# Performance work log

Measured on AMD Instinct MI355X. Metric: run time of the kernel, lower is better.

## Reference

```python
import jax, jax.numpy as jnp
import numpy as np

B, T, C, H = 2, 2048, 2048, 32
N = C // H  # 64
EPS_GN = 1e-5 * 8 ** 2  # eps = 1e-5 * head_size_divisor**2


def setup_inputs() -> dict:
    key = jax.random.key(0)
    ks = jax.random.split(key, 40)
    p = lambda i, shape, s=1.0: jax.random.normal(ks[i], shape, jnp.float32) * s
    inp = {
        'x': p(0, (B, T, C)),
        'shift_state': jnp.zeros((B, C), jnp.float32),
        'v_first': p(1, (B, T, C)),
        'wkv_state': jnp.zeros((B, H, N, N), jnp.float32),
        # token-shift mix coefficients [1,1,C]
        'x_r': p(2, (1, 1, C), 0.3), 'x_w': p(3, (1, 1, C), 0.3),
        'x_k': p(4, (1, 1, C), 0.3), 'x_v': p(5, (1, 1, C), 0.3),
        'x_a': p(6, (1, 1, C), 0.3), 'x_g': p(7, (1, 1, C), 0.3),
        # decay LoRA
        'w0': p(8, (1, 1, C), 0.5) - 4.0,
        'w1': p(9, (C, 64), 0.02), 'w2': p(10, (64, C), 0.02),
        # in-context-learning-rate LoRA
        'a0': p(11, (1, 1, C), 0.1),
        'a1': p(12, (C, 64), 0.02), 'a2': p(13, (64, C), 0.02),
        # value-mix LoRA
        'v0': p(14, (1, 1, C), 0.1) + 1.0,
        'v1': p(15, (C, 32), 0.02), 'v2': p(16, (32, C), 0.02),
        # gate LoRA
        'g1': p(17, (C, 128), 0.02), 'g2': p(18, (128, C), 0.02),
        'k_k': p(19, (1, 1, C), 0.05) + 0.85,
        'k_a': p(20, (1, 1, C), 0.05) + 1.0,
        'r_k': p(21, (H, N), 0.1),
        # dense projections (applied as x @ W.T like nn.Linear)
        'Wr': p(22, (C, C), 0.02), 'Wk': p(23, (C, C), 0.02),
        'Wv': p(24, (C, C), 0.02), 'Wo': p(25, (C, C), 0.02),
        'ln_w': jnp.ones((C,), jnp.float32),
        'ln_b': jnp.zeros((C,), jnp.float32),
    }
    return inp


def reference(x, shift_state, v_first, wkv_state, x_r, x_w, x_k, x_v, x_a, x_g,
              w0, w1, w2, a0, a1, a2, v0, v1, v2, g1, g2, k_k, k_a, r_k,
              Wr, Wk, Wv, Wo, ln_w, ln_b):
    # token shift: xx[t] = x[t-1] - x[t] (prev from shift_state at t=0)
    xx = jnp.concatenate([shift_state[:, None, :], x[:, :-1]], axis=1) - x
    xr, xw, xk, xv, xa, xg = (x + xx * m for m in (x_r, x_w, x_k, x_v, x_a, x_g))

    r = xr @ Wr.T
    w = -jax.nn.softplus(-(w0 + jnp.tanh(xw @ w1) @ w2)) - 0.5  # log-decay in (-inf,-0.5)
    k = xk @ Wk.T
    v = xv @ Wv.T
    v = v + (v_first - v) * jax.nn.sigmoid(v0 + (xv @ v1) @ v2)  # layer_id > 0 branch
    a = jax.nn.sigmoid(a0 + (xa @ a1) @ a2)
    g = jax.nn.sigmoid(xg @ g1) @ g2

    kk = (k * k_k).reshape(B, T, H, N)
    kk = kk / jnp.maximum(jnp.linalg.norm(kk, axis=-1, keepdims=True), 1e-12)
    kk = kk.reshape(B, T, C)
    k = k * (1.0 + (a - 1.0) * k_a)

    # RWKV-7 generalized delta-rule recurrence (a_in=-kk, b_in=kk*a):
    #   S_t = S_{t-1} * diag(exp(w_t)) + (S_{t-1} a_t) b_t^T + v_t k_t^T ; o_t = S_t r_t
    to_tbhn = lambda z: z.reshape(B, T, H, N).transpose(1, 0, 2, 3)  # [T,B,H,N]
    rs, ws, ks, vs, as_, bs = map(to_tbhn, (r, w, k, v, -kk, kk * a))

    def step(S, ins):  # S: [B,H,N,N] indexed [v_dim, k_dim]
        r_t, w_t, k_t, v_t, a_t, b_t = ins
        sa = jnp.einsum('bhij,bhj->bhi', S, a_t)
        S = (S * jnp.exp(w_t)[:, :, None, :]
             + sa[..., None] * b_t[:, :, None, :]
             + v_t[..., None] * k_t[:, :, None, :])
        o_t = jnp.einsum('bhij,bhj->bhi', S, r_t)
        return S, o_t

    _, o = jax.lax.scan(step, wkv_state, (rs, ws, ks, vs, as_, bs))  # o: [T,B,H,N]
    o = o.transpose(1, 0, 2, 3).reshape(B, T, C)

    # GroupNorm with H groups over channel dim
    og = o.reshape(B, T, H, N)
    mu = og.mean(-1, keepdims=True)
    var = og.var(-1, keepdims=True)
    o = ((og - mu) / jnp.sqrt(var + EPS_GN)).reshape(B, T, C) * ln_w + ln_b

    # bonus term
    rk = (r.reshape(B, T, H, N) * k.reshape(B, T, H, N) * r_k).sum(-1, keepdims=True)
    o = o + (rk * v.reshape(B, T, H, N)).reshape(B, T, C)

    return (o * g) @ Wo.T
```

## Files before the change

kernel.cpp:

```cpp
#include <hip/hip_runtime.h>

#define Bdim 2
#define Tdim 2048
#define Cdim 2048
#define Hdim 32
#define Mdim (Bdim*Tdim)

typedef unsigned short u16;
typedef short bf16x8 __attribute__((ext_vector_type(8)));
typedef float f32x4 __attribute__((ext_vector_type(4)));

__device__ __forceinline__ u16 f2bf(float f) {
  unsigned u = __float_as_uint(f);
  u = (u + 0x7FFFu + ((u >> 16) & 1u)) >> 16;
  return (u16)u;
}
__device__ __forceinline__ float b2f(u16 h) {
  return __uint_as_float(((unsigned)h) << 16);
}
__device__ __forceinline__ float sigf(float x) { return 1.f / (1.f + expf(-x)); }

__device__ __forceinline__ void gld16(const u16* g, u16* l) {
  __builtin_amdgcn_global_load_lds(
      (const __attribute__((address_space(1))) unsigned int*)g,
      (__attribute__((address_space(3))) unsigned int*)l, 16, 0, 0);
}

__device__ __forceinline__ float dpp_red8(float x) {
  int t = __builtin_amdgcn_mov_dpp(__float_as_int(x), 0xB1, 0xF, 0xF, true);
  x += __int_as_float(t);
  t = __builtin_amdgcn_mov_dpp(__float_as_int(x), 0x4E, 0xF, 0xF, true);
  x += __int_as_float(t);
  t = __builtin_amdgcn_mov_dpp(__float_as_int(x), 0x128, 0xF, 0xF, true);
  x += __int_as_float(t);
  return x;
}

__global__ __launch_bounds__(256) void fill_kernel(float* __restrict__ out, float v, int n) {
  int i = blockIdx.x * 256 + threadIdx.x;
  if (i < n) out[i] = v;
}

__global__ __launch_bounds__(256) void prep_kernel(
    const float* __restrict__ x, const float* __restrict__ shift,
    const float* __restrict__ mr, const float* __restrict__ mw,
    const float* __restrict__ mk, const float* __restrict__ mv,
    const float* __restrict__ ma, const float* __restrict__ mg,
    u16* __restrict__ xr_h, u16* __restrict__ xr_l,
    u16* __restrict__ xk_h, u16* __restrict__ xk_l,
    u16* __restrict__ xv_h, u16* __restrict__ xv_l,
    u16* __restrict__ xg_h, u16* __restrict__ xg_l,
    u16* __restrict__ xw, u16* __restrict__ xa)
{
  size_t idx = (size_t)blockIdx.x * 256 + threadIdx.x;
  int c = (int)(idx & (Cdim - 1));
  size_t row = idx >> 11;
  int t = (int)(row & (Tdim - 1));
  int b = (int)(row >> 11);
  float xc = x[idx];
  float xp = (t == 0) ? shift[(size_t)b * Cdim + c] : x[idx - Cdim];
  float xx = xp - xc;

  float vr = xc + xx * mr[c];
  u16 hr = f2bf(vr); xr_h[idx] = hr; xr_l[idx] = f2bf(vr - b2f(hr));
  float vk = xc + xx * mk[c];
  u16 hk = f2bf(vk); xk_h[idx] = hk; xk_l[idx] = f2bf(vk - b2f(hk));
  float vv = xc + xx * mv[c];
  u16 hv = f2bf(vv); xv_h[idx] = hv; xv_l[idx] = f2bf(vv - b2f(hv));
  float vg = xc + xx * mg[c];
  u16 hg = f2bf(vg); xg_h[idx] = hg; xg_l[idx] = f2bf(vg - b2f(hg));

  xw[idx] = f2bf(xc + xx * mw[c]);
  xa[idx] = f2bf(xc + xx * ma[c]);
}

__global__ __launch_bounds__(256) void cast_split_kernel(
    const float* __restrict__ src, u16* __restrict__ hi, u16* __restrict__ lo)
{
  size_t i = (size_t)blockIdx.x * 256 + threadIdx.x;
  float v = src[i];
  u16 h = f2bf(v);
  hi[i] = h;
  lo[i] = f2bf(v - b2f(h));
}

__global__ __launch_bounds__(256) void transpose_pack_kernel(
    const float* __restrict__ src, u16* __restrict__ dst, int K, int Nsrc)
{
  size_t idx = (size_t)blockIdx.x * 256 + threadIdx.x;
  int n = (int)(idx / K);
  int kk = (int)(idx - (size_t)n * K);
  dst[idx] = (n < Nsrc) ? f2bf(src[(size_t)kk * Nsrc + n]) : (u16)0;
}

__global__ __launch_bounds__(256) void transpose_pack_split_kernel(
    const float* __restrict__ src, u16* __restrict__ dh, u16* __restrict__ dl,
    int K, int Nsrc)
{
  size_t idx = (size_t)blockIdx.x * 256 + threadIdx.x;
  int n = (int)(idx / K);
  int kk = (int)(idx - (size_t)n * K);
  float v = (n < Nsrc) ? src[(size_t)kk * Nsrc + n] : 0.f;
  u16 h = f2bf(v);
  dh[idx] = h;
  dl[idx] = f2bf(v - b2f(h));
}


template <int EP>
__device__ __forceinline__ void gemm_plain_body(
    const u16* __restrict__ A, const u16* __restrict__ B, void* __restrict__ Cv,
    const float* __restrict__ bias, const float* __restrict__ aux1,
    const float* __restrict__ aux2, int K, int Nact, int ldC, int act)
{
  __shared__ u16 As[128][32];
  __shared__ u16 Bs[128][32];
  int tid = threadIdx.x;
  int lane = tid & 63, wave = tid >> 6;
  int wm = wave >> 1, wn = wave & 1;
  int bm = blockIdx.x * 128, bn = blockIdx.y * 128;
  f32x4 zero = {0.f, 0.f, 0.f, 0.f};
  f32x4 acc[4][4];
#pragma unroll
  for (int i = 0; i < 4; i++)
#pragma unroll
    for (int j = 0; j < 4; j++) acc[i][j] = zero;
  int srow = tid >> 2;
  int sslot = tid & 3;
  int scol = (sslot ^ (srow & 3)) << 3;
  int dcol = sslot << 3;
  const u16* gA  = A + (size_t)(bm + srow) * K + scol;
  const u16* gA2 = A + (size_t)(bm + 64 + srow) * K + scol;
  const u16* gB  = B + (size_t)(bn + srow) * K + scol;
  const u16* gB2 = B + (size_t)(bn + 64 + srow) * K + scol;
  u16* lA  = &As[srow][dcol];
  u16* lA2 = &As[64 + srow][dcol];
  u16* lB  = &Bs[srow][dcol];
  u16* lB2 = &Bs[64 + srow][dcol];
  int fr = lane & 15;
  int fk = ((lane >> 4) << 3) ^ ((fr & 3) << 3);
  for (int k0 = 0; k0 < K; k0 += 32) {
    __syncthreads();
    gld16(gA + k0, lA);
    gld16(gA2 + k0, lA2);
    gld16(gB + k0, lB);
    gld16(gB2 + k0, lB2);
    __syncthreads();
    bf16x8 af[4], bfv[4];
#pragma unroll
    for (int i = 0; i < 4; i++) af[i] = *(const bf16x8*)&As[wm * 64 + i * 16 + fr][fk];
#pragma unroll
    for (int j = 0; j < 4; j++) bfv[j] = *(const bf16x8*)&Bs[wn * 64 + j * 16 + fr][fk];
#pragma unroll
    for (int i = 0; i < 4; i++)
#pragma unroll
      for (int j = 0; j < 4; j++)
        acc[i][j] = __builtin_amdgcn_mfma_f32_16x16x32_bf16(af[i], bfv[j], acc[i][j], 0, 0, 0);
  }
  int rb = (lane >> 4) << 2;
  int cc = lane & 15;
#pragma unroll
  for (int i = 0; i < 4; i++) {
    int mm = bm + wm * 64 + i * 16 + rb;
#pragma unroll
    for (int j = 0; j < 4; j++) {
      int nn = bn + wn * 64 + j * 16 + cc;
      if (nn < Nact) {
#pragma unroll
        for (int r = 0; r < 4; r++) {
          float val = acc[i][j][r];
          size_t oidx = (size_t)(mm + r) * ldC + nn;
          if (EP == 1) ((u16*)Cv)[oidx] = f2bf(tanhf(val));
          else if (EP == 2) {
            if (act == 1) val = tanhf(val);
            ((u16*)Cv)[oidx] = f2bf(val);
          }
          else if (EP == 3) ((u16*)Cv)[oidx] = f2bf(0.60653065971f * sigf(bias[nn] + val));
          else if (EP == 4) ((float*)Cv)[oidx] = sigf(bias[nn] + val);
          else if (EP == 5) {
            float vraw = aux1[oidx], vf = aux2[oidx];
            ((float*)Cv)[oidx] = vraw + (vf - vraw) * sigf(bias[nn] + val);
          }
        }
      }
    }
  }
}

template <int EP>
__global__ __launch_bounds__(256) void gemm_plain(
    const u16* __restrict__ A, const u16* __restrict__ B, void* __restrict__ C,
    const float* __restrict__ bias, const float* __restrict__ aux1,
    const float* __restrict__ aux2, int K, int Nact, int ldC)
{
  gemm_plain_body<EP>(A, B, C, bias, aux1, aux2, K, Nact, ldC, 0);
}

__global__ __launch_bounds__(256) void lora1_kernel(
    const u16* A0, const u16* A1, const u16* A2,
    const u16* B0, const u16* B1, const u16* B2,
    u16* C0, u16* C1, u16* C2, int N0, int N1, int N2)
{
  int z = blockIdx.z;
  const u16* A = (z == 0) ? A0 : (z == 1) ? A1 : A2;
  const u16* B = (z == 0) ? B0 : (z == 1) ? B1 : B2;
  u16* C      = (z == 0) ? C0 : (z == 1) ? C1 : C2;
  int Nact    = (z == 0) ? N0 : (z == 1) ? N1 : N2;
  int act     = (z == 0) ? 1 : 0;
  gemm_plain_body<2>(A, B, C, nullptr, nullptr, nullptr, 2048, Nact, Nact, act);
}

template <int EP>
__global__ __launch_bounds__(256) void gemm_split(
    const u16* __restrict__ Ah, const u16* __restrict__ Al,
    const u16* __restrict__ Bh, const u16* __restrict__ Bl,
    void* __restrict__ C1, u16* __restrict__ C2, int K, int Nact, int ldC)
{
  __shared__ u16 Ash[128][32];
  __shared__ u16 Asl[128][32];
  __shared__ u16 Bsh[128][32];
  __shared__ u16 Bsl[128][32];
  int tid = threadIdx.x;
  int lane = tid & 63, wave = tid >> 6;
  int wm = wave >> 1, wn = wave & 1;
  int bm = blockIdx.x * 128, bn = blockIdx.y * 128;
  f32x4 zero = {0.f, 0.f, 0.f, 0.f};
  f32x4 acc[4][4];
#pragma unroll
  for (int i = 0; i < 4; i++)
#pragma unroll
    for (int j = 0; j < 4; j++) acc[i][j] = zero;
  int srow = tid >> 2;
  int sslot = tid & 3;
  int scol = (sslot ^ (srow & 3)) << 3;
  int dcol = sslot << 3;
  size_t ga  = (size_t)(bm + srow) * K + scol;
  size_t ga2 = (size_t)(bm + 64 + srow) * K + scol;
  size_t gb  = (size_t)(bn + srow) * K + scol;
  size_t gb2 = (size_t)(bn + 64 + srow) * K + scol;
  u16* lAh = &Ash[srow][dcol];  u16* lAh2 = &Ash[64 + srow][dcol];
  u16* lAl = &Asl[srow][dcol];  u16* lAl2 = &Asl[64 + srow][dcol];
  u16* lBh = &Bsh[srow][dcol];  u16* lBh2 = &Bsh[64 + srow][dcol];
  u16* lBl = &Bsl[srow][dcol];  u16* lBl2 = &Bsl[64 + srow][dcol];
  int fr = lane & 15;
  int fk = ((lane >> 4) << 3) ^ ((fr & 3) << 3);
  for (int k0 = 0; k0 < K; k0 += 32) {
    __syncthreads();
    gld16(Ah + ga + k0, lAh);
    gld16(Ah + ga2 + k0, lAh2);
    gld16(Al + ga + k0, lAl);
    gld16(Al + ga2 + k0, lAl2);
    gld16(Bh + gb + k0, lBh);
    gld16(Bh + gb2 + k0, lBh2);
    gld16(Bl + gb + k0, lBl);
    gld16(Bl + gb2 + k0, lBl2);
    __syncthreads();
    bf16x8 fah[4], fal[4], fbh[4], fbl[4];
#pragma unroll
    for (int i = 0; i < 4; i++) {
      fah[i] = *(const bf16x8*)&Ash[wm * 64 + i * 16 + fr][fk];
      fal[i] = *(const bf16x8*)&Asl[wm * 64 + i * 16 + fr][fk];
    }
#pragma unroll
    for (int j = 0; j < 4; j++) {
      fbh[j] = *(const bf16x8*)&Bsh[wn * 64 + j * 16 + fr][fk];
      fbl[j] = *(const bf16x8*)&Bsl[wn * 64 + j * 16 + fr][fk];
    }
#pragma unroll
    for (int i = 0; i < 4; i++)
#pragma unroll
      for (int j = 0; j < 4; j++) {
        acc[i][j] = __builtin_amdgcn_mfma_f32_16x16x32_bf16(fah[i], fbh[j], acc[i][j], 0, 0, 0);
        acc[i][j] = __builtin_amdgcn_mfma_f32_16x16x32_bf16(fah[i], fbl[j], acc[i][j], 0, 0, 0);
        acc[i][j] = __builtin_amdgcn_mfma_f32_16x16x32_bf16(fal[i], fbh[j], acc[i][j], 0, 0, 0);
      }
  }
  int rb = (lane >> 4) << 2;
  int cc = lane & 15;
#pragma unroll
  for (int i = 0; i < 4; i++) {
    int mm = bm + wm * 64 + i * 16 + rb;
#pragma unroll
    for (int j = 0; j < 4; j++) {
      int nn = bn + wn * 64 + j * 16 + cc;
      if (nn < Nact) {
#pragma unroll
        for (int r = 0; r < 4; r++) {
          float val = acc[i][j][r];
          size_t oidx = (size_t)(mm + r) * ldC + nn;
          if (EP == 0) ((float*)C1)[oidx] = val;
          else {
            float s = sigf(val);
            u16 h = f2bf(s);
            ((u16*)C1)[oidx] = h;
            C2[oidx] = f2bf(s - b2f(h));
          }
        }
      }
    }
  }
}

__global__ __launch_bounds__(256) void post_kernel(
    float* __restrict__ k, const float* __restrict__ a,
    const float* __restrict__ k_k, const float* __restrict__ k_a,
    float* __restrict__ ain, float* __restrict__ bin)
{
  int gid = blockIdx.x * 4 + (threadIdx.x >> 6);
  int lane = threadIdx.x & 63;
  int m = gid >> 5, h = gid & 31;
  int c = h * 64 + lane;
  size_t idx = (size_t)m * Cdim + c;

  float kr = k[idx];
  float av = a[idx];

  float kkv = kr * k_k[c];
  float ss = kkv * kkv;
#pragma unroll
  for (int off = 32; off; off >>= 1) ss += __shfl_xor(ss, off);
  float kkn = kkv / fmaxf(sqrtf(ss), 1e-12f);

  ain[idx] = -kkn;
  bin[idx] = kkn * av;
  k[idx] = kr * (1.f + (av - 1.f) * k_a[c]);
}

__global__ __launch_bounds__(64) void scan_kernel(
    const float* __restrict__ r, const u16* __restrict__ ew,
    const float* __restrict__ k, const float* __restrict__ v,
    const float* __restrict__ ain, const float* __restrict__ bin,
    const float* __restrict__ S0, float* __restrict__ o)
{
  int bh = blockIdx.x & 63;
  int rg = blockIdx.x >> 6;
  int lane = threadIdx.x;
  int oc = (lane & 3) | ((lane >> 1) & 4);
  int lr = ((lane >> 2) & 1) | ((lane >> 3) & 6);
  int i = rg * 8 + lr;
  int cb = (bh & 31) * 64;
  size_t mbase = (size_t)(bh >> 5) * Tdim;

  float s[8];
  {
    const float* sp = S0 + (size_t)bh * 4096 + (size_t)i * 64 + oc * 8;
#pragma unroll
    for (int j = 0; j < 8; j++) s[j] = sp[j];
  }

  __shared__ __align__(16) char ring[33792];
  char* RA = ring;
  char* RK = ring + 6144;
  char* RB = ring + 12288;
  char* RR = ring + 18432;
  char* RE = ring + 24576;
  char* RV = ring + 27648;

  int lhi = lane >> 4, llo = lane & 15;
  int ehi = lane >> 3, elo = lane & 7;

#define STAGE(gg) { \
  int ss_ = (gg) % 3; \
  size_t m0_ = mbase + (size_t)(gg) * 8; \
  gld16((const u16*)(ain + (m0_ + lhi) * Cdim + cb + llo * 4),     (u16*)(RA + ss_ * 2048)); \
  gld16((const u16*)(ain + (m0_ + 4 + lhi) * Cdim + cb + llo * 4), (u16*)(RA + ss_ * 2048 + 1024)); \
  gld16((const u16*)(k   + (m0_ + lhi) * Cdim + cb + llo * 4),     (u16*)(RK + ss_ * 2048)); \
  gld16((const u16*)(k   + (m0_ + 4 + lhi) * Cdim + cb + llo * 4), (u16*)(RK + ss_ * 2048 + 1024)); \
  gld16((const u16*)(bin + (m0_ + lhi) * Cdim + cb + llo * 4),     (u16*)(RB + ss_ * 2048)); \
  gld16((const u16*)(bin + (m0_ + 4 + lhi) * Cdim + cb + llo * 4), (u16*)(RB + ss_ * 2048 + 1024)); \
  gld16((const u16*)(r   + (m0_ + lhi) * Cdim + cb + llo * 4),     (u16*)(RR + ss_ * 2048)); \
  gld16((const u16*)(r   + (m0_ + 4 + lhi) * Cdim + cb + llo * 4), (u16*)(RR + ss_ * 2048 + 1024)); \
  gld16((const u16*)(v   + (m0_ + lhi) * Cdim + cb + llo * 4),     (u16*)(RV + ss_ * 2048)); \
  gld16((const u16*)(v   + (m0_ + 4 + lhi) * Cdim + cb + llo * 4), (u16*)(RV + ss_ * 2048 + 1024)); \
  gld16((const u16*)(ew  + (m0_ + ehi) * Cdim + cb + elo * 8),     (u16*)(RE + ss_ * 1024)); }

  f32x4 aA0, aA1, kA0, kA1, bA0, bA1, rA0, rA1;
  f32x4 aB0, aB1, kB0, kB1, bB0, bB1, rB0, rB1;
  f32x4 aC0, aC1, kC0, kC1, bC0, bC1, rC0, rC1;
  bf16x8 eA, eB, eC;
  float vA, vB, vC;

#define LOADSUB(sub, a0_, a1_, k0_, k1_, b0_, b1_, r0_, r1_, e_, v_) { \
  const f32x4* pa_ = (const f32x4*)(RA + ssoff + (sub) * 256 + oc * 32); \
  a0_ = pa_[0]; a1_ = pa_[1]; \
  const f32x4* pk_ = (const f32x4*)(RK + ssoff + (sub) * 256 + oc * 32); \
  k0_ = pk_[0]; k1_ = pk_[1]; \
  const f32x4* pb_ = (const f32x4*)(RB + ssoff + (sub) * 256 + oc * 32); \
  b0_ = pb_[0]; b1_ = pb_[1]; \
  const f32x4* pr_ = (const f32x4*)(RR + ssoff + (sub) * 256 + oc * 32); \
  r0_ = pr_[0]; r1_ = pr_[1]; \
  e_ = *(const bf16x8*)(RE + (ssoff >> 1) + (sub) * 128 + oc * 16); \
  v_ = *(const float*)(RV + ssoff + (sub) * 256 + i * 4); }

#define COMPSUB(sub, a0_, a1_, k0_, k1_, b0_, b1_, r0_, r1_, e_, v_) { \
  float pL_ = 0.f, pH_ = 0.f; \
  _Pragma("unroll") \
  for (int j = 0; j < 4; j++) { pL_ += s[j] * a0_[j]; pH_ += s[4 + j] * a1_[j]; } \
  float p_ = dpp_red8(pL_ + pH_); \
  float oL_ = 0.f, oH_ = 0.f; \
  _Pragma("unroll") \
  for (int j = 0; j < 4; j++) { \
    float sn0_ = s[j]     * b2f((u16)e_[j])     + p_ * b0_[j] + v_ * k0_[j]; \
    float sn1_ = s[4 + j] * b2f((u16)e_[4 + j]) + p_ * b1_[j] + v_ * k1_[j]; \
    s[j] = sn0_; s[4 + j] = sn1_; \
    oL_ += sn0_ * r0_[j]; oH_ += sn1_ * r1_[j]; \
  } \
  float oo_ = dpp_red8(oL_ + oH_); \
  if (oc == 0) o[(mbase + (size_t)g * 8 + (sub)) * Cdim + cb + i] = oo_; }

#define LA(sub) LOADSUB(sub, aA0, aA1, kA0, kA1, bA0, bA1, rA0, rA1, eA, vA)
#define LB(sub) LOADSUB(sub, aB0, aB1, kB0, kB1, bB0, bB1, rB0, rB1, eB, vB)
#define LC(sub) LOADSUB(sub, aC0, aC1, kC0, kC1, bC0, bC1, rC0, rC1, eC, vC)
#define CA(sub) COMPSUB(sub, aA0, aA1, kA0, kA1, bA0, bA1, rA0, rA1, eA, vA)
#define CB(sub) COMPSUB(sub, aB0, aB1, kB0, kB1, bB0, bB1, rB0, rB1, eB, vB)
#define CC(sub) COMPSUB(sub, aC0, aC1, kC0, kC1, bC0, bC1, rC0, rC1, eC, vC)

  const int NG = Tdim / 8;
  STAGE(0)
  STAGE(1)

  for (int g = 0; g < NG; ++g) {
    if (g + 2 < NG) STAGE(g + 2)
    if (g + 1 < NG) asm volatile("s_waitcnt vmcnt(22)" ::: "memory");
    else            asm volatile("s_waitcnt vmcnt(0)" ::: "memory");
    __builtin_amdgcn_sched_barrier(0);
    int ssoff = (g % 3) * 2048;
    LA(0)
    LB(1)
    LC(2)
    CA(0)
    LA(3)
    CB(1)
    LB(4)
    CC(2)
    LC(5)
    CA(3)
    LA(6)
    CB(4)
    LB(7)
    CC(5)
    CA(6)
    CB(7)
  }
#undef STAGE
#undef LOADSUB
#undef COMPSUB
#undef LA
#undef LB
#undef LC
#undef CA
#undef CB
#undef CC
}

__global__ __launch_bounds__(256) void gn_kernel(
    const float* __restrict__ o_raw, const float* __restrict__ r,
    const float* __restrict__ k, const float* __restrict__ v,
    const float* __restrict__ g, const float* __restrict__ rkw,
    const float* __restrict__ ln_w, const float* __restrict__ ln_b,
    u16* __restrict__ og_h, u16* __restrict__ og_l)
{
  int gid = blockIdx.x * 4 + (threadIdx.x >> 6);
  int lane = threadIdx.x & 63;
  int m = gid >> 5, h = gid & 31;
  int c = h * 64 + lane;
  size_t idx = (size_t)m * Cdim + c;

  float ov = o_raw[idx];
  float rv = r[idx], kv = k[idx], vv = v[idx];
  float rk = rv * kv * rkw[c];

  float s1 = ov, s2 = ov * ov, s3 = rk;
#pragma unroll
  for (int off = 32; off; off >>= 1) {
    s1 += __shfl_xor(s1, off);
    s2 += __shfl_xor(s2, off);
    s3 += __shfl_xor(s3, off);
  }
  float mu = s1 * (1.f / 64.f);
  float var = s2 * (1.f / 64.f) - mu * mu;
  float xh = (ov - mu) * rsqrtf(var + 6.4e-4f);
  float gn = xh * ln_w[c] + ln_b[c];
  float outp = (gn + s3 * vv) * g[idx];
  u16 hh = f2bf(outp);
  og_h[idx] = hh;
  og_l[idx] = f2bf(outp - b2f(hh));
}

extern "C" void kernel_launch(void* const* d_in, const int* in_sizes, int n_in,
                              void* d_out, int out_size, void* d_ws, size_t ws_size,
                              hipStream_t stream) {
  const float* x      = (const float*)d_in[0];
  const float* shiftS = (const float*)d_in[1];
  const float* vfirst = (const float*)d_in[2];
  const float* wkv0   = (const float*)d_in[3];
  const float* x_r = (const float*)d_in[4];
  const float* x_w = (const float*)d_in[5];
  const float* x_k = (const float*)d_in[6];
  const float* x_v = (const float*)d_in[7];
  const float* x_a = (const float*)d_in[8];
  const float* x_g = (const float*)d_in[9];
  const float* w0 = (const float*)d_in[10];
  const float* w1 = (const float*)d_in[11];
  const float* w2 = (const float*)d_in[12];
  const float* a0 = (const float*)d_in[13];
  const float* a1 = (const float*)d_in[14];
  const float* a2 = (const float*)d_in[15];
  const float* v0 = (const float*)d_in[16];
  const float* v1 = (const float*)d_in[17];
  const float* v2 = (const float*)d_in[18];
  const float* g1 = (const float*)d_in[19];
  const float* g2 = (const float*)d_in[20];
  const float* k_k = (const float*)d_in[21];
  const float* k_a = (const float*)d_in[22];
  const float* r_k = (const float*)d_in[23];
  const float* Wr = (const float*)d_in[24];
  const float* Wk = (const float*)d_in[25];
  const float* Wv = (const float*)d_in[26];
  const float* Wo = (const float*)d_in[27];
  const float* ln_w = (const float*)d_in[28];
  const float* ln_b = (const float*)d_in[29];
  (void)in_sizes; (void)n_in;

  const size_t MC = (size_t)Mdim * Cdim;
  const size_t CC = (size_t)Cdim * Cdim;
  const size_t SLOT = MC * 2;

  char* cur = (char*)d_ws;
  auto alloc = [&](size_t bytes) -> void* {
    void* p = cur;
    cur += (bytes + 255) & ~(size_t)255;
    return p;
  };

  char* X = (char*)alloc(13 * SLOT);
  u16* xr_h = (u16*)(X + 0 * SLOT);
  u16* xr_l = (u16*)(X + 1 * SLOT);
  u16* xk_h = (u16*)(X + 2 * SLOT);
  u16* xk_l = (u16*)(X + 3 * SLOT);
  u16* xv_h = (u16*)(X + 4 * SLOT);
  u16* xv_l = (u16*)(X + 5 * SLOT);
  u16* xw   = (u16*)(X + 6 * SLOT);
  u16* xa   = (u16*)(X + 7 * SLOT);
  u16* xg_h = (u16*)(X + 8 * SLOT);
  u16* xg_l = (u16*)(X + 9 * SLOT);
  float* r_f32 = (float*)(X + 8 * SLOT);
  float* k_f32 = (float*)(X + 0 * SLOT);
  float* v_f32 = (float*)(X + 2 * SLOT);
  float* a_f32 = (float*)(X + 10 * SLOT);
  u16*   ew_bf = (u16*)(X + 12 * SLOT);
  float* ain_f = (float*)(X + 4 * SLOT);
  float* bin_f = (float*)(X + 6 * SLOT);
  float* o_f32 = (float*)(X + 10 * SLOT);
  float* g_f32 = (float*)(X + 6 * SLOT);
  u16*   og_h  = (u16*)(X + 4 * SLOT);
  u16*   og_l  = (u16*)(X + 5 * SLOT);

  u16* Wh = (u16*)alloc(CC * 2);
  u16* Wl = (u16*)alloc(CC * 2);

  u16* w1t = (u16*)alloc((size_t)128 * 2048 * 2);
  u16* a1t = (u16*)alloc((size_t)128 * 2048 * 2);
  u16* v1t = (u16*)alloc((size_t)128 * 2048 * 2);
  u16* g1t_h = (u16*)alloc((size_t)128 * 2048 * 2);
  u16* g1t_l = (u16*)alloc((size_t)128 * 2048 * 2);
  u16* w2t = (u16*)alloc((size_t)2048 * 64 * 2);
  u16* a2t = (u16*)alloc((size_t)2048 * 64 * 2);
  u16* v2t = (u16*)alloc((size_t)2048 * 32 * 2);
  u16* g2t_h = (u16*)alloc((size_t)2048 * 128 * 2);
  u16* g2t_l = (u16*)alloc((size_t)2048 * 128 * 2);
  u16* hb_w = (u16*)alloc((size_t)Mdim * 64 * 2);
  u16* hb_a = (u16*)alloc((size_t)Mdim * 64 * 2);
  u16* hb_v = (u16*)alloc((size_t)Mdim * 32 * 2);
  u16* sig_h = (u16*)alloc((size_t)Mdim * 128 * 2);
  u16* sig_l = (u16*)alloc((size_t)Mdim * 128 * 2);

  size_t required = (size_t)(cur - (char*)d_ws);
  if (ws_size < required) {
    fill_kernel<<<(out_size + 255) / 256, 256, 0, stream>>>(
        (float*)d_out, (float)(ws_size >> 20), out_size);
    return;
  }

  prep_kernel<<<(int)(MC / 256), 256, 0, stream>>>(
      x, shiftS, x_r, x_w, x_k, x_v, x_a, x_g,
      xr_h, xr_l, xk_h, xk_l, xv_h, xv_l, xg_h, xg_l, xw, xa);

  transpose_pack_kernel<<<1024, 256, 0, stream>>>(w1, w1t, 2048, 64);
  transpose_pack_kernel<<<1024, 256, 0, stream>>>(a1, a1t, 2048, 64);
  transpose_pack_kernel<<<1024, 256, 0, stream>>>(v1, v1t, 2048, 32);
  transpose_pack_split_kernel<<<1024, 256, 0, stream>>>(g1, g1t_h, g1t_l, 2048, 128);
  transpose_pack_kernel<<<512, 256, 0, stream>>>(w2, w2t, 64, 2048);
  transpose_pack_kernel<<<512, 256, 0, stream>>>(a2, a2t, 64, 2048);
  transpose_pack_kernel<<<256, 256, 0, stream>>>(v2, v2t, 32, 2048);
  transpose_pack_split_kernel<<<1024, 256, 0, stream>>>(g2, g2t_h, g2t_l, 128, 2048);

  dim3 gL1(Mdim / 128, 1, 3);
  lora1_kernel<<<gL1, 256, 0, stream>>>(xw, xa, xv_h, w1t, a1t, v1t,
                                        hb_w, hb_a, hb_v, 64, 64, 32);
  dim3 gL1g(Mdim / 128, 1);
  gemm_split<1><<<gL1g, 256, 0, stream>>>(xg_h, xg_l, g1t_h, g1t_l,
                                          sig_h, sig_l, 2048, 128, 128);

  dim3 gBig(Mdim / 128, Cdim / 128);
  cast_split_kernel<<<(int)(CC / 256), 256, 0, stream>>>(Wr, Wh, Wl);
  gemm_split<0><<<gBig, 256, 0, stream>>>(xr_h, xr_l, Wh, Wl, r_f32, nullptr, Cdim, Cdim, Cdim);
  cast_split_kernel<<<(int)(CC / 256), 256, 0, stream>>>(Wk, Wh, Wl);
  gemm_split<0><<<gBig, 256, 0, stream>>>(xk_h, xk_l, Wh, Wl, k_f32, nullptr, Cdim, Cdim, Cdim);
  cast_split_kernel<<<(int)(CC / 256), 256, 0, stream>>>(Wv, Wh, Wl);
  gemm_split<0><<<gBig, 256, 0, stream>>>(xv_h, xv_l, Wh, Wl, v_f32, nullptr, Cdim, Cdim, Cdim);

  gemm_plain<3><<<gBig, 256, 0, stream>>>(hb_w, w2t, ew_bf, w0, nullptr, nullptr, 64, Cdim, Cdim);
  gemm_plain<4><<<gBig, 256, 0, stream>>>(hb_a, a2t, a_f32, a0, nullptr, nullptr, 64, Cdim, Cdim);
  gemm_plain<5><<<gBig, 256, 0, stream>>>(hb_v, v2t, v_f32, v0, v_f32, vfirst, 32, Cdim, Cdim);

  post_kernel<<<(Mdim * Hdim) / 4, 256, 0, stream>>>(
      k_f32, a_f32, k_k, k_a, ain_f, bin_f);

  scan_kernel<<<512, 64, 0, stream>>>(
      r_f32, ew_bf, k_f32, v_f32, ain_f, bin_f, wkv0, o_f32);

  gemm_split<0><<<gBig, 256, 0, stream>>>(sig_h, sig_l, g2t_h, g2t_l,
                                          g_f32, nullptr, 128, Cdim, Cdim);

  gn_kernel<<<(Mdim * Hdim) / 4, 256, 0, stream>>>(
      o_f32, r_f32, k_f32, v_f32, g_f32, r_k, ln_w, ln_b, og_h, og_l);

  cast_split_kernel<<<(int)(CC / 256), 256, 0, stream>>>(Wo, Wh, Wl);
  gemm_split<0><<<gBig, 256, 0, stream>>>(og_h, og_l, Wh, Wl,
                                          (float*)d_out, nullptr, Cdim, Cdim, Cdim);
}
```

Baseline: 1.169 ms.

## Load A fragments and scan inputs directly from global into registers, dropping LDS staging

In the split-precision GEMM, the A operand fragments are now read straight from global memory into registers instead of being staged through shared memory; only B still goes through LDS. In the WKV scan kernel, the three-slot LDS ring fed by async global-to-LDS loads is replaced by direct per-timestep register prefetch, kept four timesteps ahead in a software pipeline. The aim is to cut LDS traffic, the waitcnt and sync overhead, and LDS occupancy. The cost is that global-load latency is hidden only by register prefetch depth, and the GEMM's uncoalesced strided A reads may raise memory traffic.

```diff
diff --git a/kernel.cpp b/kernel.cpp
--- a/kernel.cpp
+++ b/kernel.cpp
@@ -216,8 +216,6 @@
     const u16* __restrict__ Bh, const u16* __restrict__ Bl,
     void* __restrict__ C1, u16* __restrict__ C2, int K, int Nact, int ldC)
 {
-  __shared__ u16 Ash[128][32];
-  __shared__ u16 Asl[128][32];
   __shared__ u16 Bsh[128][32];
   __shared__ u16 Bsl[128][32];
   int tid = threadIdx.x;
@@ -234,37 +232,32 @@
   int sslot = tid & 3;
   int scol = (sslot ^ (srow & 3)) << 3;
   int dcol = sslot << 3;
-  size_t ga  = (size_t)(bm + srow) * K + scol;
-  size_t ga2 = (size_t)(bm + 64 + srow) * K + scol;
   size_t gb  = (size_t)(bn + srow) * K + scol;
   size_t gb2 = (size_t)(bn + 64 + srow) * K + scol;
-  u16* lAh = &Ash[srow][dcol];  u16* lAh2 = &Ash[64 + srow][dcol];
-  u16* lAl = &Asl[srow][dcol];  u16* lAl2 = &Asl[64 + srow][dcol];
   u16* lBh = &Bsh[srow][dcol];  u16* lBh2 = &Bsh[64 + srow][dcol];
   u16* lBl = &Bsl[srow][dcol];  u16* lBl2 = &Bsl[64 + srow][dcol];
   int fr = lane & 15;
-  int fk = ((lane >> 4) << 3) ^ ((fr & 3) << 3);
+  int fkB = ((lane >> 4) << 3) ^ ((fr & 3) << 3);
+  const u16* gAh = Ah + (size_t)(bm + wm * 64 + fr) * K + ((lane >> 4) << 3);
+  const u16* gAl = Al + (size_t)(bm + wm * 64 + fr) * K + ((lane >> 4) << 3);
   for (int k0 = 0; k0 < K; k0 += 32) {
     __syncthreads();
-    gld16(Ah + ga + k0, lAh);
-    gld16(Ah + ga2 + k0, lAh2);
-    gld16(Al + ga + k0, lAl);
-    gld16(Al + ga2 + k0, lAl2);
     gld16(Bh + gb + k0, lBh);
     gld16(Bh + gb2 + k0, lBh2);
     gld16(Bl + gb + k0, lBl);
     gld16(Bl + gb2 + k0, lBl2);
+    bf16x8 fah[4], fal[4];
+#pragma unroll
+    for (int i = 0; i < 4; i++) {
+      fah[i] = *(const bf16x8*)(gAh + (size_t)i * 16 * K + k0);
+      fal[i] = *(const bf16x8*)(gAl + (size_t)i * 16 * K + k0);
+    }
     __syncthreads();
-    bf16x8 fah[4], fal[4], fbh[4], fbl[4];
-#pragma unroll
-    for (int i = 0; i < 4; i++) {
-      fah[i] = *(const bf16x8*)&Ash[wm * 64 + i * 16 + fr][fk];
-      fal[i] = *(const bf16x8*)&Asl[wm * 64 + i * 16 + fr][fk];
-    }
+    bf16x8 fbh[4], fbl[4];
 #pragma unroll
     for (int j = 0; j < 4; j++) {
-      fbh[j] = *(const bf16x8*)&Bsh[wn * 64 + j * 16 + fr][fk];
-      fbl[j] = *(const bf16x8*)&Bsl[wn * 64 + j * 16 + fr][fk];
+      fbh[j] = *(const bf16x8*)&Bsh[wn * 64 + j * 16 + fr][fkB];
+      fbl[j] = *(const bf16x8*)&Bsl[wn * 64 + j * 16 + fr][fkB];
     }
 #pragma unroll
     for (int i = 0; i < 4; i++)
@@ -348,109 +341,63 @@
     for (int j = 0; j < 8; j++) s[j] = sp[j];
   }
 
-  __shared__ __align__(16) char ring[33792];
-  char* RA = ring;
-  char* RK = ring + 6144;
-  char* RB = ring + 12288;
-  char* RR = ring + 18432;
-  char* RE = ring + 24576;
-  char* RV = ring + 27648;
-
-  int lhi = lane >> 4, llo = lane & 15;
-  int ehi = lane >> 3, elo = lane & 7;
-
-#define STAGE(gg) { \
-  int ss_ = (gg) % 3; \
-  size_t m0_ = mbase + (size_t)(gg) * 8; \
-  gld16((const u16*)(ain + (m0_ + lhi) * Cdim + cb + llo * 4),     (u16*)(RA + ss_ * 2048)); \
-  gld16((const u16*)(ain + (m0_ + 4 + lhi) * Cdim + cb + llo * 4), (u16*)(RA + ss_ * 2048 + 1024)); \
-  gld16((const u16*)(k   + (m0_ + lhi) * Cdim + cb + llo * 4),     (u16*)(RK + ss_ * 2048)); \
-  gld16((const u16*)(k   + (m0_ + 4 + lhi) * Cdim + cb + llo * 4), (u16*)(RK + ss_ * 2048 + 1024)); \
-  gld16((const u16*)(bin + (m0_ + lhi) * Cdim + cb + llo * 4),     (u16*)(RB + ss_ * 2048)); \
-  gld16((const u16*)(bin + (m0_ + 4 + lhi) * Cdim + cb + llo * 4), (u16*)(RB + ss_ * 2048 + 1024)); \
-  gld16((const u16*)(r   + (m0_ + lhi) * Cdim + cb + llo * 4),     (u16*)(RR + ss_ * 2048)); \
-  gld16((const u16*)(r   + (m0_ + 4 + lhi) * Cdim + cb + llo * 4), (u16*)(RR + ss_ * 2048 + 1024)); \
-  gld16((const u16*)(v   + (m0_ + lhi) * Cdim + cb + llo * 4),     (u16*)(RV + ss_ * 2048)); \
-  gld16((const u16*)(v   + (m0_ + 4 + lhi) * Cdim + cb + llo * 4), (u16*)(RV + ss_ * 2048 + 1024)); \
-  gld16((const u16*)(ew  + (m0_ + ehi) * Cdim + cb + elo * 8),     (u16*)(RE + ss_ * 1024)); }
-
   f32x4 aA0, aA1, kA0, kA1, bA0, bA1, rA0, rA1;
   f32x4 aB0, aB1, kB0, kB1, bB0, bB1, rB0, rB1;
   f32x4 aC0, aC1, kC0, kC1, bC0, bC1, rC0, rC1;
-  bf16x8 eA, eB, eC;
-  float vA, vB, vC;
-
-#define LOADSUB(sub, a0_, a1_, k0_, k1_, b0_, b1_, r0_, r1_, e_, v_) { \
-  const f32x4* pa_ = (const f32x4*)(RA + ssoff + (sub) * 256 + oc * 32); \
-  a0_ = pa_[0]; a1_ = pa_[1]; \
-  const f32x4* pk_ = (const f32x4*)(RK + ssoff + (sub) * 256 + oc * 32); \
-  k0_ = pk_[0]; k1_ = pk_[1]; \
-  const f32x4* pb_ = (const f32x4*)(RB + ssoff + (sub) * 256 + oc * 32); \
-  b0_ = pb_[0]; b1_ = pb_[1]; \
-  const f32x4* pr_ = (const f32x4*)(RR + ssoff + (sub) * 256 + oc * 32); \
-  r0_ = pr_[0]; r1_ = pr_[1]; \
-  e_ = *(const bf16x8*)(RE + (ssoff >> 1) + (sub) * 128 + oc * 16); \
-  v_ = *(const float*)(RV + ssoff + (sub) * 256 + i * 4); }
-
-#define COMPSUB(sub, a0_, a1_, k0_, k1_, b0_, b1_, r0_, r1_, e_, v_) { \
+  f32x4 aD0, aD1, kD0, kD1, bD0, bD1, rD0, rD1;
+  bf16x8 eA, eB, eC, eD;
+  float vA, vB, vC, vD;
+
+#define PRE(tt, P) { \
+  size_t vb_ = (mbase + (size_t)(tt)) * Cdim + cb; \
+  const f32x4* pa_ = (const f32x4*)(ain + vb_ + oc * 8); \
+  a##P##0 = pa_[0]; a##P##1 = pa_[1]; \
+  const f32x4* pk_ = (const f32x4*)(k + vb_ + oc * 8); \
+  k##P##0 = pk_[0]; k##P##1 = pk_[1]; \
+  const f32x4* pb_ = (const f32x4*)(bin + vb_ + oc * 8); \
+  b##P##0 = pb_[0]; b##P##1 = pb_[1]; \
+  const f32x4* pr_ = (const f32x4*)(r + vb_ + oc * 8); \
+  r##P##0 = pr_[0]; r##P##1 = pr_[1]; \
+  e##P = *(const bf16x8*)(ew + vb_ + oc * 8); \
+  v##P = v[vb_ + i]; }
+
+#define COMP(tt, P) { \
   float pL_ = 0.f, pH_ = 0.f; \
   _Pragma("unroll") \
-  for (int j = 0; j < 4; j++) { pL_ += s[j] * a0_[j]; pH_ += s[4 + j] * a1_[j]; } \
+  for (int j = 0; j < 4; j++) { pL_ += s[j] * a##P##0[j]; pH_ += s[4 + j] * a##P##1[j]; } \
   float p_ = dpp_red8(pL_ + pH_); \
   float oL_ = 0.f, oH_ = 0.f; \
   _Pragma("unroll") \
   for (int j = 0; j < 4; j++) { \
-    float sn0_ = s[j]     * b2f((u16)e_[j])     + p_ * b0_[j] + v_ * k0_[j]; \
-    float sn1_ = s[4 + j] * b2f((u16)e_[4 + j]) + p_ * b1_[j] + v_ * k1_[j]; \
+    float sn0_ = s[j]     * b2f((u16)e##P[j])     + p_ * b##P##0[j] + v##P * k##P##0[j]; \
+    float sn1_ = s[4 + j] * b2f((u16)e##P[4 + j]) + p_ * b##P##1[j] + v##P * k##P##1[j]; \
     s[j] = sn0_; s[4 + j] = sn1_; \
-    oL_ += sn0_ * r0_[j]; oH_ += sn1_ * r1_[j]; \
+    oL_ += sn0_ * r##P##0[j]; oH_ += sn1_ * r##P##1[j]; \
   } \
   float oo_ = dpp_red8(oL_ + oH_); \
-  if (oc == 0) o[(mbase + (size_t)g * 8 + (sub)) * Cdim + cb + i] = oo_; }
-
-#define LA(sub) LOADSUB(sub, aA0, aA1, kA0, kA1, bA0, bA1, rA0, rA1, eA, vA)
-#define LB(sub) LOADSUB(sub, aB0, aB1, kB0, kB1, bB0, bB1, rB0, rB1, eB, vB)
-#define LC(sub) LOADSUB(sub, aC0, aC1, kC0, kC1, bC0, bC1, rC0, rC1, eC, vC)
-#define CA(sub) COMPSUB(sub, aA0, aA1, kA0, kA1, bA0, bA1, rA0, rA1, eA, vA)
-#define CB(sub) COMPSUB(sub, aB0, aB1, kB0, kB1, bB0, bB1, rB0, rB1, eB, vB)
-#define CC(sub) COMPSUB(sub, aC0, aC1, kC0, kC1, bC0, bC1, rC0, rC1, eC, vC)
-
-  const int NG = Tdim / 8;
-  STAGE(0)
-  STAGE(1)
-
-  for (int g = 0; g < NG; ++g) {
-    if (g + 2 < NG) STAGE(g + 2)
-    if (g + 1 < NG) asm volatile("s_waitcnt vmcnt(22)" ::: "memory");
-    else            asm volatile("s_waitcnt vmcnt(0)" ::: "memory");
-    __builtin_amdgcn_sched_barrier(0);
-    int ssoff = (g % 3) * 2048;
-    LA(0)
-    LB(1)
-    LC(2)
-    CA(0)
-    LA(3)
-    CB(1)
-    LB(4)
-    CC(2)
-    LC(5)
-    CA(3)
-    LA(6)
-    CB(4)
-    LB(7)
-    CC(5)
-    CA(6)
-    CB(7)
-  }
-#undef STAGE
-#undef LOADSUB
-#undef COMPSUB
-#undef LA
-#undef LB
-#undef LC
-#undef CA
-#undef CB
-#undef CC
+  if (oc == 0) o[(mbase + (size_t)(tt)) * Cdim + cb + i] = oo_; \
+  __builtin_amdgcn_sched_barrier(0); }
+
+  PRE(0, A)
+  PRE(1, B)
+  PRE(2, C)
+  for (int t = 0; t < Tdim - 4; t += 4) {
+    PRE(t + 3, D)
+    COMP(t, A)
+    PRE(t + 4, A)
+    COMP(t + 1, B)
+    PRE(t + 5, B)
+    COMP(t + 2, C)
+    PRE(t + 6, C)
+    COMP(t + 3, D)
+  }
+  PRE(Tdim - 1, D)
+  COMP(Tdim - 4, A)
+  COMP(Tdim - 3, B)
+  COMP(Tdim - 2, C)
+  COMP(Tdim - 1, D)
+#undef PRE
+#undef COMP
 }
 
 __global__ __launch_bounds__(256) void gn_kernel(
```

New measurement: 1.440 ms. 1.23x slower.
